# Kernel optimization log

Measured on AMD Instinct MI355X. Metric: run time of the kernel, lower is better.

Reference implementation:

```python
import jax, jax.numpy as jnp
import numpy as np

BN_EPS = 1e-5
NEG_SLOPE = 0.2

def _bn(x, g, b, m, v):
    # inference-mode BatchNorm1d over the channel (last) axis
    return (x - m) * jax.lax.rsqrt(v + BN_EPS) * g + b

def _lrelu(x):
    return jnp.where(x >= 0, x, NEG_SLOPE * x)

def setup_inputs() -> dict:
    key = jax.random.key(0)
    ks = jax.random.split(key, 24)
    B, N, K, Cr, Cin, Cnb, Cout = 2, 65536, 16, 10, 64, 64, 128
    Ccat = Cin + Cnb
    return {
        'xyz': jax.random.normal(ks[0], (B, N, 3), jnp.float32),
        'feature': jax.random.normal(ks[1], (B, N, Cin), jnp.float32),
        'raw_neighbors_feature': jax.random.normal(ks[2], (B, N, K, Cr), jnp.float32),
        'neighbors_idx': jax.random.randint(ks[3], (B, N, K), 0, N, jnp.int32),
        'W_nb': jax.random.normal(ks[4], (Cr, Cnb), jnp.float32) * 0.3,
        'b_nb': jax.random.normal(ks[5], (Cnb,), jnp.float32),
        'g_nb': jax.random.uniform(ks[6], (Cnb,), jnp.float32),
        'be_nb': jax.random.normal(ks[7], (Cnb,), jnp.float32),
        'm_nb': jax.random.normal(ks[8], (Cnb,), jnp.float32),
        'v_nb': jax.random.uniform(ks[9], (Cnb,), jnp.float32),
        'W_attn': jax.random.normal(ks[10], (Ccat, Ccat), jnp.float32) * 0.09,
        'W_out': jax.random.normal(ks[11], (Ccat, Cout), jnp.float32) * 0.09,
        'b_out': jax.random.normal(ks[12], (Cout,), jnp.float32),
        'g_out': jax.random.uniform(ks[13], (Cout,), jnp.float32),
        'be_out': jax.random.normal(ks[14], (Cout,), jnp.float32),
        'm_out': jax.random.normal(ks[15], (Cout,), jnp.float32),
        'v_out': jax.random.uniform(ks[16], (Cout,), jnp.float32),
        'W_sc': jax.random.normal(ks[17], (Cin, Cout), jnp.float32) * 0.12,
        'b_sc': jax.random.normal(ks[18], (Cout,), jnp.float32),
        'g_sc': jax.random.uniform(ks[19], (Cout,), jnp.float32),
        'be_sc': jax.random.normal(ks[20], (Cout,), jnp.float32),
        'm_sc': jax.random.normal(ks[21], (Cout,), jnp.float32),
        'v_sc': jax.random.uniform(ks[22], (Cout,), jnp.float32),
    }

def reference(xyz, feature, raw_neighbors_feature, neighbors_idx,
              W_nb, b_nb, g_nb, be_nb, m_nb, v_nb,
              W_attn,
              W_out, b_out, g_out, be_out, m_out, v_out,
              W_sc, b_sc, g_sc, be_sc, m_sc, v_sc):
    # mlp_neighbor_fea: Linear -> BN1d -> leaky_relu(0.2) over raw neighbor features
    nb = _lrelu(_bn(jnp.einsum('bnkc,cd->bnkd', raw_neighbors_feature, W_nb) + b_nb,
                    g_nb, be_nb, m_nb, v_nb))              # [B,N,K,Cnb]
    # index_points: gather per-point neighbor features [B,N,K,Cin]
    gathered = jax.vmap(lambda f, i: f[i])(feature, neighbors_idx)
    fea = jnp.concatenate([gathered, nb], axis=-1)          # [B,N,K,Ccat]
    # attn pooling: softmax over neighbor axis K of a bias-free linear
    attn = jax.nn.softmax(jnp.einsum('bnkc,cd->bnkd', fea, W_attn), axis=2)
    pooled = jnp.sum(attn * fea, axis=2)                    # [B,N,Ccat]
    out_branch = _bn(pooled @ W_out + b_out, g_out, be_out, m_out, v_out)
    sc_branch = _bn(feature @ W_sc + b_sc, g_sc, be_sc, m_sc, v_sc)
    return _lrelu(sc_branch + out_branch)                   # [B,N,Cout]
```

## Files before the change

kernel.cpp:

```cpp
#include <hip/hip_runtime.h>


#define KNB   16
#define CR    10
#define CIN   64
#define CCAT  128
#define COUT  128
#define NPTS  131072
#define EPS   1e-5f
#define LOG2E 1.4426950408889634f

#define WS_WB   0
#define WS_W3   32768
#define WS_WNB  81920
#define WS_B3   86016
#define WS_BNB  86528

typedef const float* fp;
typedef short bf16x8 __attribute__((ext_vector_type(8)));
typedef float f32x4  __attribute__((ext_vector_type(4)));
typedef __bf16 bf16x2 __attribute__((ext_vector_type(2)));

__device__ __forceinline__ unsigned short f2bf(float x) {
    return __builtin_bit_cast(unsigned short, (__bf16)x);
}
__device__ __forceinline__ unsigned int pack2(float a, float b) {
    bf16x2 v; v.x = (__bf16)a; v.y = (__bf16)b;
    return __builtin_bit_cast(unsigned int, v);
}
__device__ __forceinline__ float bf2f(unsigned short h) {
    return __uint_as_float(((unsigned int)h) << 16);
}
__device__ __forceinline__ float lrelu(float x) { return fmaxf(x, 0.2f * x); }

__global__ __launch_bounds__(256) void lfa_prep(
    fp W_nb, fp b_nb, fp g_nb, fp be_nb, fp m_nb, fp v_nb,
    fp W_attn,
    fp W_out, fp b_out, fp g_out, fp be_out, fp m_out, fp v_out,
    fp W_sc,  fp b_sc,  fp g_sc,  fp be_sc,  fp m_sc,  fp v_sc,
    unsigned char* __restrict__ ws)
{
    const int t = blockIdx.x * 256 + threadIdx.x;
    if (t < 2048) {
        const int n0 = t >> 8, s = (t >> 6) & 3, ln = t & 63;
        const int n = (n0 << 4) + (ln & 15);
        unsigned int v[4];
        #pragma unroll
        for (int jj = 0; jj < 4; ++jj) {
            const int k = (s << 5) + ((ln >> 4) << 3) + jj * 2;
            v[jj] = pack2(W_attn[k * CCAT + n] * LOG2E,
                          W_attn[(k + 1) * CCAT + n] * LOG2E);
        }
        *(uint4*)(ws + WS_WB + t * 16) = make_uint4(v[0], v[1], v[2], v[3]);
    } else if (t < 5120) {
        const int e = t - 2048;
        const int t8 = e / 384, rem = e % 384, s = rem >> 6, ln = rem & 63;
        const int d = (t8 << 4) + (ln & 15);
        const float so = g_out[d] * rsqrtf(v_out[d] + EPS);
        const float ss = g_sc[d]  * rsqrtf(v_sc[d]  + EPS);
        unsigned int v[4];
        #pragma unroll
        for (int jj = 0; jj < 4; ++jj) {
            float a[2];
            #pragma unroll
            for (int h = 0; h < 2; ++h) {
                const int k = (s << 5) + ((ln >> 4) << 3) + jj * 2 + h;
                a[h] = (k < CCAT) ? W_out[k * COUT + d] * so
                                  : W_sc[(k - CCAT) * COUT + d] * ss;
            }
            v[jj] = pack2(a[0], a[1]);
        }
        *(uint4*)(ws + WS_W3 + e * 16) = make_uint4(v[0], v[1], v[2], v[3]);
    } else if (t < 5376) {
        const int e = t - 5120;
        const int n0 = e >> 6, ln = e & 63;
        const int n = (n0 << 4) + (ln & 15);
        const float sn = g_nb[n] * rsqrtf(v_nb[n] + EPS);
        unsigned int v[4];
        #pragma unroll
        for (int jj = 0; jj < 4; ++jj) {
            float a[2];
            #pragma unroll
            for (int h = 0; h < 2; ++h) {
                const int k = ((ln >> 4) << 3) + jj * 2 + h;
                a[h] = (k < CR) ? W_nb[k * 64 + n] * sn : 0.f;
            }
            v[jj] = pack2(a[0], a[1]);
        }
        *(uint4*)(ws + WS_WNB + e * 16) = make_uint4(v[0], v[1], v[2], v[3]);
    } else if (t < 5504) {
        const int d = t - 5376;
        const float so = g_out[d] * rsqrtf(v_out[d] + EPS);
        const float ss = g_sc[d]  * rsqrtf(v_sc[d]  + EPS);
        ((float*)(ws + WS_B3))[d] =
              (b_out[d] - m_out[d]) * so + be_out[d]
            + (b_sc[d]  - m_sc[d])  * ss + be_sc[d];
    } else if (t < 5568) {
        const int d = t - 5504;
        const float sn = g_nb[d] * rsqrtf(v_nb[d] + EPS);
        ((float*)(ws + WS_BNB))[d] = (b_nb[d] - m_nb[d]) * sn + be_nb[d];
    }
}

__global__ __launch_bounds__(256, 2) void lfa_main(
    fp feature, fp raw, const int* __restrict__ nidx,
    const unsigned char* __restrict__ ws, float* __restrict__ out)
{
    __shared__ __align__(16) unsigned short feaA[4][16][136];
    __shared__ __align__(16) unsigned short pooledA[4][16][200];

    const int tid  = threadIdx.x;
    const int w    = tid >> 6;
    const int lane = tid & 63;
    const int quad = lane >> 4;
    const int l15  = lane & 15;
    const int p0   = (blockIdx.x * 4 + w) * 16;
    const int b    = p0 >> 16;

    bf16x8 WB[8][4];
    #pragma unroll
    for (int n0 = 0; n0 < 8; ++n0)
        #pragma unroll
        for (int s = 0; s < 4; ++s)
            WB[n0][s] = *(const bf16x8*)(ws + WS_WB + (((n0 * 4 + s) * 64 + lane) << 4));

    float binb[4];
    #pragma unroll
    for (int j = 0; j < 4; ++j)
        binb[j] = ((const float*)(ws + WS_BNB))[j * 16 + l15];

    #pragma unroll 1
    for (int it = 0; it < 8; ++it) {
        const int pp0 = p0 + it * 2;

        int idxv = 0;
        if (lane < 32) idxv = nidx[pp0 * KNB + lane];

        if (lane < 32) {
            const int pt = lane >> 4, c4 = l15 * 4;
            const float4 cf = *(const float4*)&feature[(size_t)(pp0 + pt) * CIN + c4];
            uint2 pk; pk.x = pack2(cf.x, cf.y); pk.y = pack2(cf.z, cf.w);
            *(uint2*)&pooledA[w][it * 2 + pt][CCAT + c4] = pk;
        }

        #pragma unroll
        for (int pt = 0; pt < 2; ++pt) {
            const int p = pp0 + pt;

            float4 gv[4];
            #pragma unroll
            for (int i = 0; i < 4; ++i) {
                const int ni = __shfl(idxv, pt * 16 + i * 4 + quad, 64);
                gv[i] = *(const float4*)&feature[(size_t)((b << 16) + ni) * CIN + l15 * 4];
            }

            bf16x8 anb = {0, 0, 0, 0, 0, 0, 0, 0};
            {
                const float* rp = raw + (size_t)p * (KNB * CR) + l15 * CR;
                if (quad == 0) {
                    const float2 r0 = *(const float2*)(rp + 0);
                    const float2 r1 = *(const float2*)(rp + 2);
                    const float2 r2 = *(const float2*)(rp + 4);
                    const float2 r3 = *(const float2*)(rp + 6);
                    anb[0] = (short)f2bf(r0.x); anb[1] = (short)f2bf(r0.y);
                    anb[2] = (short)f2bf(r1.x); anb[3] = (short)f2bf(r1.y);
                    anb[4] = (short)f2bf(r2.x); anb[5] = (short)f2bf(r2.y);
                    anb[6] = (short)f2bf(r3.x); anb[7] = (short)f2bf(r3.y);
                } else if (quad == 1) {
                    const float2 r4 = *(const float2*)(rp + 8);
                    anb[0] = (short)f2bf(r4.x); anb[1] = (short)f2bf(r4.y);
                }
            }

            float nbC[4][4];
            #pragma unroll
            for (int n0 = 0; n0 < 4; ++n0) {
                const bf16x8 bw = *(const bf16x8*)(ws + WS_WNB + ((n0 * 64 + lane) << 4));
                f32x4 c = {0.f, 0.f, 0.f, 0.f};
                c = __builtin_amdgcn_mfma_f32_16x16x32_bf16(anb, bw, c, 0, 0, 0);
                #pragma unroll
                for (int r = 0; r < 4; ++r) {
                    const float x = lrelu(c[r] + binb[n0]);
                    nbC[n0][r] = x;
                    feaA[w][quad * 4 + r][64 + n0 * 16 + l15] = f2bf(x);
                }
            }

            #pragma unroll
            for (int i = 0; i < 4; ++i) {
                uint2 pk; pk.x = pack2(gv[i].x, gv[i].y); pk.y = pack2(gv[i].z, gv[i].w);
                *(uint2*)&feaA[w][i * 4 + quad][l15 * 4] = pk;
            }

            bf16x8 A[4];
            #pragma unroll
            for (int s = 0; s < 4; ++s)
                A[s] = *(const bf16x8*)&feaA[w][l15][s * 32 + quad * 8];

            #pragma unroll
            for (int n0 = 0; n0 < 8; ++n0) {
                f32x4 c = {0.f, 0.f, 0.f, 0.f};
                #pragma unroll
                for (int s = 0; s < 4; ++s)
                    c = __builtin_amdgcn_mfma_f32_16x16x32_bf16(A[s], WB[n0][s], c, 0, 0, 0);
                const float e0 = __builtin_amdgcn_exp2f(c[0]);
                const float e1 = __builtin_amdgcn_exp2f(c[1]);
                const float e2 = __builtin_amdgcn_exp2f(c[2]);
                const float e3 = __builtin_amdgcn_exp2f(c[3]);
                float den = e0 + e1 + e2 + e3;
                float num;
                if (n0 < 4) {
                    num = e0 * bf2f(feaA[w][quad * 4 + 0][n0 * 16 + l15])
                        + e1 * bf2f(feaA[w][quad * 4 + 1][n0 * 16 + l15])
                        + e2 * bf2f(feaA[w][quad * 4 + 2][n0 * 16 + l15])
                        + e3 * bf2f(feaA[w][quad * 4 + 3][n0 * 16 + l15]);
                } else {
                    num = e0 * nbC[n0 - 4][0] + e1 * nbC[n0 - 4][1]
                        + e2 * nbC[n0 - 4][2] + e3 * nbC[n0 - 4][3];
                }
                num += __shfl_xor(num, 16, 64);
                den += __shfl_xor(den, 16, 64);
                num += __shfl_xor(num, 32, 64);
                den += __shfl_xor(den, 32, 64);
                const float pp = __fdividef(num, den);
                if (quad == 0)
                    pooledA[w][it * 2 + pt][n0 * 16 + l15] = f2bf(pp);
            }
        }
    }

    bf16x8 A3[6];
    #pragma unroll
    for (int s = 0; s < 6; ++s)
        A3[s] = *(const bf16x8*)&pooledA[w][l15][s * 32 + quad * 8];
    #pragma unroll
    for (int t = 0; t < 8; ++t) {
        f32x4 c = {0.f, 0.f, 0.f, 0.f};
        #pragma unroll
        for (int s = 0; s < 6; ++s) {
            const bf16x8 bw = *(const bf16x8*)(ws + WS_W3 + (((t * 6 + s) * 64 + lane) << 4));
            c = __builtin_amdgcn_mfma_f32_16x16x32_bf16(A3[s], bw, c, 0, 0, 0);
        }
        const float bz = ((const float*)(ws + WS_B3))[t * 16 + l15];
        #pragma unroll
        for (int r = 0; r < 4; ++r)
            out[(size_t)(p0 + quad * 4 + r) * COUT + t * 16 + l15] = lrelu(c[r] + bz);
    }
}

extern "C" void kernel_launch(void* const* d_in, const int* in_sizes, int n_in,
                              void* d_out, int out_size, void* d_ws, size_t ws_size,
                              hipStream_t stream)
{
    fp feature = (fp)d_in[1];
    fp raw     = (fp)d_in[2];
    const int* nidx = (const int*)d_in[3];
    fp W_nb = (fp)d_in[4],  b_nb = (fp)d_in[5],  g_nb = (fp)d_in[6];
    fp be_nb = (fp)d_in[7], m_nb = (fp)d_in[8],  v_nb = (fp)d_in[9];
    fp W_attn = (fp)d_in[10];
    fp W_out = (fp)d_in[11], b_out = (fp)d_in[12], g_out = (fp)d_in[13];
    fp be_out = (fp)d_in[14], m_out = (fp)d_in[15], v_out = (fp)d_in[16];
    fp W_sc = (fp)d_in[17], b_sc = (fp)d_in[18], g_sc = (fp)d_in[19];
    fp be_sc = (fp)d_in[20], m_sc = (fp)d_in[21], v_sc = (fp)d_in[22];

    hipLaunchKernelGGL(lfa_prep, dim3(22), dim3(256), 0, stream,
                       W_nb, b_nb, g_nb, be_nb, m_nb, v_nb,
                       W_attn,
                       W_out, b_out, g_out, be_out, m_out, v_out,
                       W_sc, b_sc, g_sc, be_sc, m_sc, v_sc,
                       (unsigned char*)d_ws);
    hipLaunchKernelGGL(lfa_main, dim3(2048), dim3(256), 0, stream,
                       feature, raw, nidx,
                       (const unsigned char*)d_ws, (float*)d_out);
}
```

Before: 418.9 us.

## Pre-convert feature table to bf16 and gather bf16 rows in main kernel

Adds a prep kernel that converts the fp32 feature table into a bf16 copy in workspace. A new main kernel then gathers neighbor features from that copy, halving gather bytes and dropping per-gather conversions. The main kernel also streams the first-stage weights from global/L1 per iteration instead of holding them in registers, which may lower register pressure. The cost is an extra pass over the feature table (32 MB read, 16 MB written), and the old path is kept as a fallback when workspace is too small.

```diff
diff --git a/kernel.cpp b/kernel.cpp
--- a/kernel.cpp
+++ b/kernel.cpp
@@ -15,6 +15,7 @@
 #define WS_WNB  81920
 #define WS_B3   86016
 #define WS_BNB  86528
+#define WS_FEA  87040
 
 typedef const float* fp;
 typedef short bf16x8 __attribute__((ext_vector_type(8)));
@@ -102,7 +103,166 @@
     }
 }
 
-__global__ __launch_bounds__(256, 2) void lfa_main(
+__global__ __launch_bounds__(256) void lfa_prep_fea(
+    fp feature, unsigned char* __restrict__ ws)
+{
+    const int t = blockIdx.x * 256 + threadIdx.x;
+    const size_t idx = (size_t)t * 8;
+    if (idx < (size_t)NPTS * CIN) {
+        const float4 f0 = *(const float4*)&feature[idx];
+        const float4 f1 = *(const float4*)&feature[idx + 4];
+        uint4 o;
+        o.x = pack2(f0.x, f0.y); o.y = pack2(f0.z, f0.w);
+        o.z = pack2(f1.x, f1.y); o.w = pack2(f1.z, f1.w);
+        *(uint4*)(ws + WS_FEA + idx * 2) = o;
+    }
+}
+
+__global__ __launch_bounds__(256, 2) void lfa_main_bf16(
+    fp raw, const int* __restrict__ nidx,
+    const unsigned char* __restrict__ ws, float* __restrict__ out)
+{
+    __shared__ __align__(16) unsigned short feaA[4][16][136];
+    __shared__ __align__(16) unsigned short pooledA[4][16][200];
+
+    const int tid  = threadIdx.x;
+    const int w    = tid >> 6;
+    const int lane = tid & 63;
+    const int quad = lane >> 4;
+    const int l15  = lane & 15;
+    const int p0   = (blockIdx.x * 4 + w) * 16;
+    const int b    = p0 >> 16;
+
+    const unsigned short* feaT = (const unsigned short*)(ws + WS_FEA);
+    const unsigned char*  wbp  = ws + WS_WB + ((size_t)lane << 4);
+
+    float binb[4];
+    #pragma unroll
+    for (int j = 0; j < 4; ++j)
+        binb[j] = ((const float*)(ws + WS_BNB))[j * 16 + l15];
+
+    #pragma unroll 1
+    for (int it = 0; it < 8; ++it) {
+        const int pp0 = p0 + it * 2;
+
+        int idxv = 0;
+        if (lane < 32) idxv = nidx[pp0 * KNB + lane];
+
+        if (lane < 32) {
+            const int pt = lane >> 4, c4 = l15 * 4;
+            const uint2 cf = *(const uint2*)&feaT[(size_t)(pp0 + pt) * CIN + c4];
+            *(uint2*)&pooledA[w][it * 2 + pt][CCAT + c4] = cf;
+        }
+
+        #pragma unroll
+        for (int pt = 0; pt < 2; ++pt) {
+            const int p = pp0 + pt;
+
+            uint2 gv[4];
+            #pragma unroll
+            for (int i = 0; i < 4; ++i) {
+                const int ni = __shfl(idxv, pt * 16 + i * 4 + quad, 64);
+                gv[i] = *(const uint2*)&feaT[(size_t)((b << 16) + ni) * CIN + l15 * 4];
+            }
+
+            bf16x8 anb = {0, 0, 0, 0, 0, 0, 0, 0};
+            {
+                const float* rp = raw + (size_t)p * (KNB * CR) + l15 * CR;
+                if (quad == 0) {
+                    const float2 r0 = *(const float2*)(rp + 0);
+                    const float2 r1 = *(const float2*)(rp + 2);
+                    const float2 r2 = *(const float2*)(rp + 4);
+                    const float2 r3 = *(const float2*)(rp + 6);
+                    anb[0] = (short)f2bf(r0.x); anb[1] = (short)f2bf(r0.y);
+                    anb[2] = (short)f2bf(r1.x); anb[3] = (short)f2bf(r1.y);
+                    anb[4] = (short)f2bf(r2.x); anb[5] = (short)f2bf(r2.y);
+                    anb[6] = (short)f2bf(r3.x); anb[7] = (short)f2bf(r3.y);
+                } else if (quad == 1) {
+                    const float2 r4 = *(const float2*)(rp + 8);
+                    anb[0] = (short)f2bf(r4.x); anb[1] = (short)f2bf(r4.y);
+                }
+            }
+
+            float nbC[4][4];
+            #pragma unroll
+            for (int n0 = 0; n0 < 4; ++n0) {
+                const bf16x8 bw = *(const bf16x8*)(ws + WS_WNB + ((n0 * 64 + lane) << 4));
+                f32x4 c = {0.f, 0.f, 0.f, 0.f};
+                c = __builtin_amdgcn_mfma_f32_16x16x32_bf16(anb, bw, c, 0, 0, 0);
+                #pragma unroll
+                for (int r = 0; r < 4; ++r) {
+                    const float x = lrelu(c[r] + binb[n0]);
+                    nbC[n0][r] = x;
+                    feaA[w][quad * 4 + r][64 + n0 * 16 + l15] = f2bf(x);
+                }
+            }
+
+            #pragma unroll
+            for (int i = 0; i < 4; ++i)
+                *(uint2*)&feaA[w][i * 4 + quad][l15 * 4] = gv[i];
+
+            bf16x8 A[4];
+            #pragma unroll
+            for (int s = 0; s < 4; ++s)
+                A[s] = *(const bf16x8*)&feaA[w][l15][s * 32 + quad * 8];
+
+            #pragma unroll
+            for (int n0 = 0; n0 < 8; ++n0) {
+                bf16x8 wb0 = *(const bf16x8*)(wbp + (n0 * 4 + 0) * 1024);
+                bf16x8 wb1 = *(const bf16x8*)(wbp + (n0 * 4 + 1) * 1024);
+                bf16x8 wb2 = *(const bf16x8*)(wbp + (n0 * 4 + 2) * 1024);
+                bf16x8 wb3 = *(const bf16x8*)(wbp + (n0 * 4 + 3) * 1024);
+                f32x4 c = {0.f, 0.f, 0.f, 0.f};
+                c = __builtin_amdgcn_mfma_f32_16x16x32_bf16(A[0], wb0, c, 0, 0, 0);
+                c = __builtin_amdgcn_mfma_f32_16x16x32_bf16(A[1], wb1, c, 0, 0, 0);
+                c = __builtin_amdgcn_mfma_f32_16x16x32_bf16(A[2], wb2, c, 0, 0, 0);
+                c = __builtin_amdgcn_mfma_f32_16x16x32_bf16(A[3], wb3, c, 0, 0, 0);
+                const float e0 = __builtin_amdgcn_exp2f(c[0]);
+                const float e1 = __builtin_amdgcn_exp2f(c[1]);
+                const float e2 = __builtin_amdgcn_exp2f(c[2]);
+                const float e3 = __builtin_amdgcn_exp2f(c[3]);
+                float den = e0 + e1 + e2 + e3;
+                float num;
+                if (n0 < 4) {
+                    num = e0 * bf2f(feaA[w][quad * 4 + 0][n0 * 16 + l15])
+                        + e1 * bf2f(feaA[w][quad * 4 + 1][n0 * 16 + l15])
+                        + e2 * bf2f(feaA[w][quad * 4 + 2][n0 * 16 + l15])
+                        + e3 * bf2f(feaA[w][quad * 4 + 3][n0 * 16 + l15]);
+                } else {
+                    num = e0 * nbC[n0 - 4][0] + e1 * nbC[n0 - 4][1]
+                        + e2 * nbC[n0 - 4][2] + e3 * nbC[n0 - 4][3];
+                }
+                num += __shfl_xor(num, 16, 64);
+                den += __shfl_xor(den, 16, 64);
+                num += __shfl_xor(num, 32, 64);
+                den += __shfl_xor(den, 32, 64);
+                const float pp = __fdividef(num, den);
+                if (quad == 0)
+                    pooledA[w][it * 2 + pt][n0 * 16 + l15] = f2bf(pp);
+            }
+        }
+    }
+
+    bf16x8 A3[6];
+    #pragma unroll
+    for (int s = 0; s < 6; ++s)
+        A3[s] = *(const bf16x8*)&pooledA[w][l15][s * 32 + quad * 8];
+    #pragma unroll
+    for (int t = 0; t < 8; ++t) {
+        f32x4 c = {0.f, 0.f, 0.f, 0.f};
+        #pragma unroll
+        for (int s = 0; s < 6; ++s) {
+            const bf16x8 bw = *(const bf16x8*)(ws + WS_W3 + (((t * 6 + s) * 64 + lane) << 4));
+            c = __builtin_amdgcn_mfma_f32_16x16x32_bf16(A3[s], bw, c, 0, 0, 0);
+        }
+        const float bz = ((const float*)(ws + WS_B3))[t * 16 + l15];
+        #pragma unroll
+        for (int r = 0; r < 4; ++r)
+            out[(size_t)(p0 + quad * 4 + r) * COUT + t * 16 + l15] = lrelu(c[r] + bz);
+    }
+}
+
+__global__ __launch_bounds__(256, 2) void lfa_main_f32(
     fp feature, fp raw, const int* __restrict__ nidx,
     const unsigned char* __restrict__ ws, float* __restrict__ out)
 {
@@ -269,7 +429,16 @@
                        W_out, b_out, g_out, be_out, m_out, v_out,
                        W_sc, b_sc, g_sc, be_sc, m_sc, v_sc,
                        (unsigned char*)d_ws);
-    hipLaunchKernelGGL(lfa_main, dim3(2048), dim3(256), 0, stream,
-                       feature, raw, nidx,
-                       (const unsigned char*)d_ws, (float*)d_out);
-}
+
+    const size_t need = (size_t)WS_FEA + (size_t)NPTS * CIN * 2;
+    if (ws_size >= need) {
+        hipLaunchKernelGGL(lfa_prep_fea, dim3(4096), dim3(256), 0, stream,
+                           feature, (unsigned char*)d_ws);
+        hipLaunchKernelGGL(lfa_main_bf16, dim3(2048), dim3(256), 0, stream,
+                           raw, nidx, (const unsigned char*)d_ws, (float*)d_out);
+    } else {
+        hipLaunchKernelGGL(lfa_main_f32, dim3(2048), dim3(256), 0, stream,
+                           feature, raw, nidx,
+                           (const unsigned char*)d_ws, (float*)d_out);
+    }
+}
```

After: 426.8 us. About the same (+1.9%).
